# Performance work log

Hardware: AMD Instinct MI355X
Metric: run time of the kernel (lower is better)

The kernel has to match this reference:

```python
import jax, jax.numpy as jnp
import numpy as np

CODEBOOK_SIZE = 1024
EMBEDDING_DIM = 64


def setup_inputs() -> dict:
    key = jax.random.key(0)
    k_in, k_cb = jax.random.split(key)
    # latent feature (batch, embedding_dim, length)
    input = jax.random.normal(k_in, (16, EMBEDDING_DIM, 8192), dtype=jnp.float32)
    # learned codebook table (codebook_size, embedding_dim)
    codebook = jax.random.normal(k_cb, (CODEBOOK_SIZE, EMBEDDING_DIM), dtype=jnp.float32)
    return {"input": input, "codebook": codebook}


def reference(input, codebook):
    # input: (B, D, T); codebook: (K, D)
    B, D = input.shape[0], input.shape[1]
    spatial = input.shape[2:]
    # move embedding dim last and flatten tokens: (B*T, D)
    x = jnp.moveaxis(input, 1, -1).reshape(-1, D)
    x_sq = jnp.sum(x * x, axis=-1, keepdims=True)            # (N, 1)
    e_sq = jnp.sum(codebook * codebook, axis=-1)             # (K,)
    dist = x_sq - 2.0 * (x @ codebook.T) + e_sq[None, :]     # (N, K)
    indices = jnp.argmin(dist, axis=-1)                      # (N,)
    quantized = jnp.take(codebook, indices, axis=0)          # (N, D)
    # reshape back: output (B, D, *spatial), indices (B, *spatial)
    out = jnp.moveaxis(quantized.reshape((B,) + spatial + (D,)), -1, 1)
    idx = indices.reshape((B,) + spatial)
    return out, idx
```

## Files before the change

kernel.cpp:

```cpp
#include <hip/hip_runtime.h>
#include <float.h>

#define K_CODES 1024
#define DIM 64
#define T_LEN 8192
#define N_TOK 131072
#define LO_SCALE 2048.0f

typedef _Float16 half8 __attribute__((ext_vector_type(8)));
typedef float    f32x4 __attribute__((ext_vector_type(4)));

#define MFMA16(a, b, c) __builtin_amdgcn_mfma_f32_16x16x32_f16((a), (b), (c), 0, 0, 0)

__global__ void vq_prep(const float* __restrict__ cb,
                        _Float16* __restrict__ w,
                        float* __restrict__ wesq) {
    __shared__ float part[128];
    const int ct   = blockIdx.x;
    const int r    = threadIdx.x;
    const int halF = r >> 7;
    const int rr   = r & 127;
    const int q    = rr >> 4;
    const int code = rr & 15;

    const float* src = cb + (size_t)(ct * 16 + code) * DIM + q * 8;
    float4 v0 = *reinterpret_cast<const float4*>(src);
    float4 v1 = *reinterpret_cast<const float4*>(src + 4);
    float x[8] = {v0.x, v0.y, v0.z, v0.w, v1.x, v1.y, v1.z, v1.w};

    half8 o;
    float psum = 0.0f;
    #pragma unroll
    for (int j = 0; j < 8; ++j) {
        _Float16 h = (_Float16)x[j];
        o[j] = halF ? (_Float16)((x[j] - (float)h) * LO_SCALE) : h;
        psum = fmaf(x[j], x[j], psum);
    }
    *reinterpret_cast<half8*>(w + (size_t)ct * 2048 + halF * 1024 + q * 128 + code * 8) = o;

    if (halF == 0) part[rr] = psum;
    __syncthreads();
    if (r < 16) {
        float s = 0.0f;
        #pragma unroll
        for (int q2 = 0; q2 < 8; ++q2) s += part[q2 * 16 + r];
        wesq[ct * 16 + r] = s * LO_SCALE;
    }
}

__global__ __launch_bounds__(256, 2)
void vq_main(const float* __restrict__ in,
             const float* __restrict__ cb,
             const _Float16* __restrict__ w,
             const float* __restrict__ wesq,
             float* __restrict__ out) {
    __shared__ float esq_s[K_CODES];
    __shared__ int   idx_s[256];

    const int tid  = threadIdx.x;
    const int wave = tid >> 6;
    const int lane = tid & 63;
    const int lo4  = lane & 15;
    const int quad = lane >> 4;

    for (int k = tid; k < K_CODES; k += 256) esq_s[k] = wesq[k];
    __syncthreads();

    const int strip = blockIdx.x * 256 + wave * 64;
    const int b  = strip >> 13;
    const int t0 = strip & 8191;

    const float* xin = in + (size_t)b * DIM * T_LEN + t0;
    half8 a_h[4][2], a_hs[4][2], a_l[4][2];
    #pragma unroll
    for (int mt = 0; mt < 4; ++mt) {
        #pragma unroll
        for (int s = 0; s < 2; ++s) {
            half8 hh, hs, ll;
            #pragma unroll
            for (int j = 0; j < 8; ++j) {
                const int d = s * 32 + quad * 8 + j;
                float xv = -2.0f * xin[(size_t)d * T_LEN + mt * 16 + lo4];
                _Float16 h = (_Float16)xv;
                hh[j] = h;
                hs[j] = (_Float16)((float)h * LO_SCALE);
                ll[j] = (_Float16)((xv - (float)h) * LO_SCALE);
            }
            a_h[mt][s] = hh;
            a_hs[mt][s] = hs;
            a_l[mt][s] = ll;
        }
    }

    float best[16];
    int   bidx[16];
    #pragma unroll
    for (int i = 0; i < 16; ++i) { best[i] = FLT_MAX; bidx[i] = 0; }

    const _Float16* wb = w + (size_t)lane * 8;

    half8 Ah0, Ah1, Al0, Al1, Bh0, Bh1, Bl0, Bl1;
    float Ae, Be;
    auto loadB = [&](int ct, half8& h0, half8& h1, half8& l0, half8& l1, float& es) {
        const _Float16* p = wb + (size_t)ct * 2048;
        h0 = *reinterpret_cast<const half8*>(p);
        h1 = *reinterpret_cast<const half8*>(p + 512);
        l0 = *reinterpret_cast<const half8*>(p + 1024);
        l1 = *reinterpret_cast<const half8*>(p + 1536);
        es = esq_s[ct * 16 + lo4];
    };
    auto step = [&](const half8& h0, const half8& h1, const half8& l0,
                    const half8& l1, float es, int ct) {
        const int code = ct * 16 + lo4;
        f32x4 c0 = {es, es, es, es}, c1 = {es, es, es, es};
        f32x4 c2 = {es, es, es, es}, c3 = {es, es, es, es};
        c0 = MFMA16(a_hs[0][0], h0, c0);
        c1 = MFMA16(a_hs[1][0], h0, c1);
        c2 = MFMA16(a_hs[2][0], h0, c2);
        c3 = MFMA16(a_hs[3][0], h0, c3);
        c0 = MFMA16(a_hs[0][1], h1, c0);
        c1 = MFMA16(a_hs[1][1], h1, c1);
        c2 = MFMA16(a_hs[2][1], h1, c2);
        c3 = MFMA16(a_hs[3][1], h1, c3);
        c0 = MFMA16(a_h[0][0], l0, c0);
        c1 = MFMA16(a_h[1][0], l0, c1);
        c2 = MFMA16(a_h[2][0], l0, c2);
        c3 = MFMA16(a_h[3][0], l0, c3);
        c0 = MFMA16(a_h[0][1], l1, c0);
        c1 = MFMA16(a_h[1][1], l1, c1);
        c2 = MFMA16(a_h[2][1], l1, c2);
        c3 = MFMA16(a_h[3][1], l1, c3);
        c0 = MFMA16(a_l[0][0], h0, c0);
        c1 = MFMA16(a_l[1][0], h0, c1);
        c2 = MFMA16(a_l[2][0], h0, c2);
        c3 = MFMA16(a_l[3][0], h0, c3);
        c0 = MFMA16(a_l[0][1], h1, c0);
        c1 = MFMA16(a_l[1][1], h1, c1);
        c2 = MFMA16(a_l[2][1], h1, c2);
        c3 = MFMA16(a_l[3][1], h1, c3);
        f32x4 cc[4] = {c0, c1, c2, c3};
        #pragma unroll
        for (int mt = 0; mt < 4; ++mt) {
            #pragma unroll
            for (int r = 0; r < 4; ++r) {
                float sc = cc[mt][r];
                const int i = mt * 4 + r;
                bool lt = sc < best[i];
                best[i] = lt ? sc : best[i];
                bidx[i] = lt ? code : bidx[i];
            }
        }
    };

    loadB(0, Ah0, Ah1, Al0, Al1, Ae);
    loadB(1, Bh0, Bh1, Bl0, Bl1, Be);
    for (int p = 0; p < 31; ++p) {
        step(Ah0, Ah1, Al0, Al1, Ae, 2 * p);
        loadB(2 * p + 2, Ah0, Ah1, Al0, Al1, Ae);
        step(Bh0, Bh1, Bl0, Bl1, Be, 2 * p + 1);
        loadB(2 * p + 3, Bh0, Bh1, Bl0, Bl1, Be);
    }
    step(Ah0, Ah1, Al0, Al1, Ae, 62);
    step(Bh0, Bh1, Bl0, Bl1, Be, 63);

    #pragma unroll
    for (int i = 0; i < 16; ++i) {
        float s = best[i];
        int  ix = bidx[i];
        #pragma unroll
        for (int off = 1; off < 16; off <<= 1) {
            float s2 = __shfl_xor(s, off, 64);
            int  ix2 = __shfl_xor(ix, off, 64);
            bool take = (s2 < s) || (s2 == s && ix2 < ix);
            s  = take ? s2 : s;
            ix = take ? ix2 : ix;
        }
        if (lo4 == 0) {
            idx_s[wave * 64 + (i >> 2) * 16 + quad * 4 + (i & 3)] = ix;
        }
    }
    __syncthreads();

    const int token = blockIdx.x * 256 + tid;
    const int tb = token >> 13;
    const int tt = token & 8191;
    const int my_idx = idx_s[tid];

    out[(size_t)N_TOK * DIM + token] = (float)my_idx;

    const float* crow = cb + (size_t)my_idx * DIM;
    float* outv = out + (size_t)tb * DIM * T_LEN + tt;
    #pragma unroll
    for (int d0 = 0; d0 < DIM; d0 += 4) {
        float4 v = *reinterpret_cast<const float4*>(crow + d0);
        outv[(size_t)(d0 + 0) * T_LEN] = v.x;
        outv[(size_t)(d0 + 1) * T_LEN] = v.y;
        outv[(size_t)(d0 + 2) * T_LEN] = v.z;
        outv[(size_t)(d0 + 3) * T_LEN] = v.w;
    }
}

extern "C" void kernel_launch(void* const* d_in, const int* in_sizes, int n_in,
                              void* d_out, int out_size, void* d_ws, size_t ws_size,
                              hipStream_t stream) {
    const float* in = (const float*)d_in[0];
    const float* cb = (const float*)d_in[1];
    float* out = (float*)d_out;

    _Float16* w   = (_Float16*)d_ws;
    float*   wesq = (float*)((char*)d_ws + 64 * 4096);

    vq_prep<<<dim3(64), dim3(256), 0, stream>>>(cb, w, wesq);
    vq_main<<<dim3(N_TOK / 256), dim3(256), 0, stream>>>(in, cb, w, wesq, out);
}
```

Measured before the change: 128.7 us.

## Stage codebook tiles through LDS ring with async global_load_lds pipeline

Replaces per-wave register double-buffered global loads of the split-half codebook with a 4-slot LDS ring filled cooperatively by global_load_lds, so each tile is fetched once per block instead of once per wave. Loads run three tiles ahead, gated by vmcnt waits and block barriers. It also raises wave priority around the MFMA chain and staggers odd blocks with s_sleep. The cost is a block-wide barrier per tile and LDS reads in place of direct register loads.

```diff
diff --git a/kernel.cpp b/kernel.cpp
--- a/kernel.cpp
+++ b/kernel.cpp
@@ -54,6 +54,7 @@
              const _Float16* __restrict__ w,
              const float* __restrict__ wesq,
              float* __restrict__ out) {
+    __shared__ __align__(16) _Float16 ring[4 * 2048];
     __shared__ float esq_s[K_CODES];
     __shared__ int   idx_s[256];
 
@@ -65,6 +66,18 @@
 
     for (int k = tid; k < K_CODES; k += 256) esq_s[k] = wesq[k];
     __syncthreads();
+
+    if (blockIdx.x & 1) __builtin_amdgcn_s_sleep(8);
+
+    auto stage = [&](int t) {
+        const char* gsrc = (const char*)w + ((size_t)t << 12) + (wave << 10) + (lane << 4);
+        _Float16* ldst = &ring[((t & 3) << 11) + (wave << 9)];
+        __builtin_amdgcn_global_load_lds(
+            (const __attribute__((address_space(1))) unsigned int*)gsrc,
+            (__attribute__((address_space(3))) unsigned int*)ldst,
+            16, 0, 0);
+    };
+    stage(0); stage(1); stage(2);
 
     const int strip = blockIdx.x * 256 + wave * 64;
     const int b  = strip >> 13;
@@ -97,23 +110,19 @@
     #pragma unroll
     for (int i = 0; i < 16; ++i) { best[i] = FLT_MAX; bidx[i] = 0; }
 
-    const _Float16* wb = w + (size_t)lane * 8;
-
-    half8 Ah0, Ah1, Al0, Al1, Bh0, Bh1, Bl0, Bl1;
-    float Ae, Be;
-    auto loadB = [&](int ct, half8& h0, half8& h1, half8& l0, half8& l1, float& es) {
-        const _Float16* p = wb + (size_t)ct * 2048;
-        h0 = *reinterpret_cast<const half8*>(p);
-        h1 = *reinterpret_cast<const half8*>(p + 512);
-        l0 = *reinterpret_cast<const half8*>(p + 1024);
-        l1 = *reinterpret_cast<const half8*>(p + 1536);
-        es = esq_s[ct * 16 + lo4];
-    };
-    auto step = [&](const half8& h0, const half8& h1, const half8& l0,
-                    const half8& l1, float es, int ct) {
-        const int code = ct * 16 + lo4;
+    const _Float16* rl = ring + (size_t)lane * 8;
+
+    auto step = [&](int t, int B) {
+        const _Float16* p = rl + B * 2048;
+        half8 h0 = *reinterpret_cast<const half8*>(p);
+        half8 h1 = *reinterpret_cast<const half8*>(p + 512);
+        half8 l0 = *reinterpret_cast<const half8*>(p + 1024);
+        half8 l1 = *reinterpret_cast<const half8*>(p + 1536);
+        float es = esq_s[t * 16 + lo4];
+        const int code = t * 16 + lo4;
         f32x4 c0 = {es, es, es, es}, c1 = {es, es, es, es};
         f32x4 c2 = {es, es, es, es}, c3 = {es, es, es, es};
+        __builtin_amdgcn_s_setprio(1);
         c0 = MFMA16(a_hs[0][0], h0, c0);
         c1 = MFMA16(a_hs[1][0], h0, c1);
         c2 = MFMA16(a_hs[2][0], h0, c2);
@@ -138,6 +147,7 @@
         c1 = MFMA16(a_l[1][1], h1, c1);
         c2 = MFMA16(a_l[2][1], h1, c2);
         c3 = MFMA16(a_l[3][1], h1, c3);
+        __builtin_amdgcn_s_setprio(0);
         f32x4 cc[4] = {c0, c1, c2, c3};
         #pragma unroll
         for (int mt = 0; mt < 4; ++mt) {
@@ -152,16 +162,23 @@
         }
     };
 
-    loadB(0, Ah0, Ah1, Al0, Al1, Ae);
-    loadB(1, Bh0, Bh1, Bl0, Bl1, Be);
-    for (int p = 0; p < 31; ++p) {
-        step(Ah0, Ah1, Al0, Al1, Ae, 2 * p);
-        loadB(2 * p + 2, Ah0, Ah1, Al0, Al1, Ae);
-        step(Bh0, Bh1, Bl0, Bl1, Be, 2 * p + 1);
-        loadB(2 * p + 3, Bh0, Bh1, Bl0, Bl1, Be);
-    }
-    step(Ah0, Ah1, Al0, Al1, Ae, 62);
-    step(Bh0, Bh1, Bl0, Bl1, Be, 63);
+#define PHASE(N)                                          \
+    asm volatile("s_waitcnt vmcnt(" #N ")" ::: "memory"); \
+    __builtin_amdgcn_s_barrier();                         \
+    __builtin_amdgcn_sched_barrier(0);
+
+    for (int q = 0; q < 15; ++q) {
+        const int t = q * 4;
+        PHASE(2) stage(t + 3); step(t, 0);
+        PHASE(2) stage(t + 4); step(t + 1, 1);
+        PHASE(2) stage(t + 5); step(t + 2, 2);
+        PHASE(2) stage(t + 6); step(t + 3, 3);
+    }
+    PHASE(2) stage(63); step(60, 0);
+    PHASE(2)            step(61, 1);
+    PHASE(1)            step(62, 2);
+    PHASE(0)            step(63, 3);
+#undef PHASE
 
     #pragma unroll
     for (int i = 0; i < 16; ++i) {
```

After: 136.2 us. 1.06x slower.
